# Performance work log

Measured on AMD Instinct MI355X. Metric: run time of the kernel, lower is better.

The kernel has to match this reference:

```python
import jax, jax.numpy as jnp
import numpy as np

# Problem sizes
P = 4096            # number of distinct property ids (segment domain)
N = 16_777_216      # number of value tokens in batch

# PropertyLossTracker hyperparameters (from __init__ defaults)
POWER = 0.5
EMA_DECAY = 0.99
MIN_FREQ = 1e-5
WARMUP_BATCHES = 1000
SLOW_WARMUP = 3000
MAX_WEIGHT = 30.0
RAMP_BATCHES = 200


def setup_inputs() -> dict:
    key = jax.random.key(0)
    k1, k2, k3 = jax.random.split(key, 3)
    property_ids = jax.random.randint(k1, (N,), 0, P)
    # CE-like nonnegative per-token losses
    token_losses = jax.random.uniform(k2, (N,), dtype=jnp.float32) * 5.0
    # EMA frequency state (dense vector replacing the defaultdict)
    prop_freq = jax.random.uniform(k3, (P,), dtype=jnp.float32) * 0.01 + MIN_FREQ
    return {
        "property_ids": property_ids,
        "token_losses": token_losses,
        "prop_freq": prop_freq,
        "batch_counter": 5000,  # > slow_warmup: steady-state weighting branch
    }


def reference(property_ids, token_losses, prop_freq, batch_counter):
    # --- fused segment reductions (replaces python loop over unique ids) ---
    ones = jnp.ones_like(token_losses)
    counts = jax.ops.segment_sum(ones, property_ids, num_segments=P)          # [P]
    sums = jax.ops.segment_sum(token_losses, property_ids, num_segments=P)    # [P]
    present = counts > 0
    # per-property mean loss (masked segment-mean)
    mean_loss = jnp.where(present, sums / jnp.maximum(counts, 1.0), 0.0)

    # --- EMA frequency update (decay all, add batch freq for present props) ---
    n_tokens = jnp.asarray(token_losses.shape[0], dtype=jnp.float32)
    batch_freq = counts / (n_tokens + 1e-6)
    new_freq = prop_freq * EMA_DECAY + jnp.where(present, (1.0 - EMA_DECAY) * batch_freq, 0.0)

    # --- inverse-frequency weights ---
    freq_cl = jnp.maximum(new_freq, MIN_FREQ)
    raw = 1.0 / (freq_cl + 1e-6) ** POWER
    ramp = jnp.minimum(1.0, (batch_counter - WARMUP_BATCHES) / RAMP_BATCHES)
    raw = 1.0 + ramp * (raw - 1.0)
    raw = jnp.minimum(MAX_WEIGHT, raw)
    # slow-warmup blend branch
    frac = batch_counter / SLOW_WARMUP
    raw = jnp.where(batch_counter <= SLOW_WARMUP, raw * frac + (1.0 - frac), raw)
    raw = jnp.where(batch_counter <= WARMUP_BATCHES, 1.0, raw)

    w = jnp.where(present, raw, 0.0)
    w = w / (w.sum() + 1e-6)

    stratified_loss = (mean_loss * w).sum()
    unweighted_loss = token_losses.mean()
    return stratified_loss, unweighted_loss, new_freq
```

## Files before the change

### kernel.cpp

```cpp
#include <hip/hip_runtime.h>

#define NPROP 4096
#define NTOK  16777216
#define BLOCK 256
#define NWAVES (BLOCK / 64)
#define GRID  512
#define NREP  8
#define STRIDE (GRID * BLOCK)
#define ROUNDS (NTOK / 4 / STRIDE)

#define TAG_SH 24
#define DATA_MASK 0x00FFFFFFu
#define CNT_SH 16
#define CNT_MASK 0xFFu
#define SUM_MASK 0xFFFFu
#define FXP_SCALE 32.0f
#define INV_FXP   (1.0f / 32.0f)

#define CSHIFT64 39
#define SUM_MASK64 ((1ULL << CSHIFT64) - 1)


__global__ __launch_bounds__(BLOCK) void hist_kernel(
    const int* __restrict__ ids, const float* __restrict__ losses,
    unsigned long long* __restrict__ g_rep)
{
    __shared__ unsigned s_hist[NWAVES * NPROP];
    for (int i = threadIdx.x; i < NWAVES * NPROP; i += BLOCK) s_hist[i] = 0u;
    __syncthreads();

    const int lane = threadIdx.x & 63;
    const int wave = threadIdx.x >> 6;
    unsigned* h = s_hist + wave * NPROP;

    const int4*   ids4 = (const int4*)ids;
    const float4* ls4  = (const float4*)losses;
    const int tid = blockIdx.x * BLOCK + threadIdx.x;

    int4   id = ids4[tid];
    float4 l  = ls4[tid];

    for (int b = 0; b < ROUNDS; ++b) {
        int nb = (b + 1) & (ROUNDS - 1);
        int4   idn = ids4[tid + nb * STRIDE];
        float4 ln  = ls4[tid + nb * STRIDE];

        int      bin[4] = { id.x, id.y, id.z, id.w };
        float    lv[4]  = { l.x,  l.y,  l.z,  l.w };
        unsigned contrib[4], tag[4], cur[4];

#pragma unroll
        for (int u = 0; u < 4; ++u) {
            contrib[u] = (1u << CNT_SH) | (unsigned)(lv[u] * FXP_SCALE + 0.5f);
            tag[u] = ((unsigned)((lane << 2) | u)) << TAG_SH;
            cur[u] = h[bin[u]];
        }

        unsigned pend = 0xFu;
        while (__any(pend != 0u)) {
#pragma unroll
            for (int u = 0; u < 4; ++u)
                if (pend & (1u << u))
                    h[bin[u]] = ((cur[u] & DATA_MASK) + contrib[u]) | tag[u];
#pragma unroll
            for (int u = 0; u < 4; ++u)
                if (pend & (1u << u)) {
                    unsigned chk = *(volatile unsigned*)&h[bin[u]];
                    if ((chk >> TAG_SH) == (tag[u] >> TAG_SH)) pend &= ~(1u << u);
                    else cur[u] = chk;
                }
        }

        id = idn; l = ln;
    }
    __syncthreads();

    unsigned long long* rep = g_rep + (unsigned)(blockIdx.x & (NREP - 1)) * NPROP;
    for (int i = threadIdx.x; i < NPROP; i += BLOCK) {
        unsigned c = 0, s = 0;
#pragma unroll
        for (int w = 0; w < NWAVES; ++w) {
            unsigned v = s_hist[w * NPROP + i];
            c += (v >> CNT_SH) & CNT_MASK;
            s += v & SUM_MASK;
        }
        if (c) atomicAdd(&rep[i], ((unsigned long long)c << CSHIFT64) | (unsigned long long)s);
    }
}

__global__ __launch_bounds__(1024) void finalize_kernel(
    const unsigned long long* __restrict__ g_rep,
    const float* __restrict__ prop_freq, const int* __restrict__ d_bc,
    float* __restrict__ out)
{
    __shared__ float s_raw[16], s_dot[16], s_tot[16];

    const int bc_i = d_bc[0];
    const float bc = (float)bc_i;
    const float ramp = fminf(1.0f, (bc - 1000.0f) / 200.0f);
    const float frac = bc / 3000.0f;

    float a_raw = 0.0f, a_dot = 0.0f, a_tot = 0.0f;

    for (int p = threadIdx.x; p < NPROP; p += 1024) {
        unsigned long long v = 0;
#pragma unroll
        for (int r = 0; r < NREP; ++r)
            v += g_rep[r * NPROP + p];

        float cnt  = (float)(unsigned)(v >> CSHIFT64);
        float sumf = (float)(v & SUM_MASK64) * INV_FXP;
        bool present = cnt > 0.0f;
        a_tot += sumf;

        float mean_loss = present ? sumf / fmaxf(cnt, 1.0f) : 0.0f;
        float batch_freq = cnt / ((float)NTOK + 1e-6f);
        float new_freq = prop_freq[p] * 0.99f + (present ? 0.01f * batch_freq : 0.0f);
        out[2 + p] = new_freq;

        float freq_cl = fmaxf(new_freq, 1e-5f);
        float raw = 1.0f / sqrtf(freq_cl + 1e-6f);
        raw = 1.0f + ramp * (raw - 1.0f);
        raw = fminf(30.0f, raw);
        if (bc_i <= 3000) raw = raw * frac + (1.0f - frac);
        if (bc_i <= 1000) raw = 1.0f;

        float w = present ? raw : 0.0f;
        a_raw += w;
        a_dot += mean_loss * w;
    }

    for (int off = 32; off > 0; off >>= 1) {
        a_raw += __shfl_down(a_raw, off, 64);
        a_dot += __shfl_down(a_dot, off, 64);
        a_tot += __shfl_down(a_tot, off, 64);
    }
    int wv = threadIdx.x >> 6;
    if ((threadIdx.x & 63) == 0) {
        s_raw[wv] = a_raw;
        s_dot[wv] = a_dot;
        s_tot[wv] = a_tot;
    }
    __syncthreads();
    if (threadIdx.x == 0) {
        float t_raw = 0.0f, t_dot = 0.0f, t_tot = 0.0f;
        for (int i = 0; i < 16; ++i) {
            t_raw += s_raw[i];
            t_dot += s_dot[i];
            t_tot += s_tot[i];
        }
        out[0] = t_dot / (t_raw + 1e-6f);
        out[1] = t_tot / (float)NTOK;
    }
}

extern "C" void kernel_launch(void* const* d_in, const int* in_sizes, int n_in,
                              void* d_out, int out_size, void* d_ws, size_t ws_size,
                              hipStream_t stream) {
    const int*   ids       = (const int*)d_in[0];
    const float* losses    = (const float*)d_in[1];
    const float* prop_freq = (const float*)d_in[2];
    const int*   d_bc      = (const int*)d_in[3];
    float* out = (float*)d_out;

    unsigned long long* g_rep = (unsigned long long*)d_ws;

    hipMemsetAsync(d_ws, 0, (size_t)NREP * NPROP * 8, stream);

    hist_kernel<<<GRID, BLOCK, 0, stream>>>(ids, losses, g_rep);
    finalize_kernel<<<1, 1024, 0, stream>>>(g_rep, prop_freq, d_bc, out);
}
```

Measured before the change: 178.4 us.

## Replace tagged-retry LDS loop with single attempt plus global atomic fallback

Each lane now writes its tagged update to the per-wave LDS histogram once and reads it back. Lanes whose write lost to another lane in the same wave send their contribution straight to the global replica with a 64-bit atomicAdd, so the wave-wide retry loop is gone. The load prefetch also deepens from one round ahead to two. This removes divergence and repeated LDS round trips on intra-wave bin collisions, at the cost of occasional global atomics and extra registers for the second prefetch buffer.

```diff
diff --git a/kernel.cpp b/kernel.cpp
--- a/kernel.cpp
+++ b/kernel.cpp
@@ -32,50 +32,49 @@
     const int lane = threadIdx.x & 63;
     const int wave = threadIdx.x >> 6;
     unsigned* h = s_hist + wave * NPROP;
+    unsigned long long* rep = g_rep + (unsigned)(blockIdx.x & (NREP - 1)) * NPROP;
 
     const int4*   ids4 = (const int4*)ids;
     const float4* ls4  = (const float4*)losses;
     const int tid = blockIdx.x * BLOCK + threadIdx.x;
 
-    int4   id = ids4[tid];
-    float4 l  = ls4[tid];
+    int4   idA = ids4[tid];
+    float4 lA  = ls4[tid];
+    int4   idB = ids4[tid + STRIDE];
+    float4 lB  = ls4[tid + STRIDE];
 
     for (int b = 0; b < ROUNDS; ++b) {
-        int nb = (b + 1) & (ROUNDS - 1);
-        int4   idn = ids4[tid + nb * STRIDE];
-        float4 ln  = ls4[tid + nb * STRIDE];
+        int nb = (b + 2) & (ROUNDS - 1);
+        int4   idC = ids4[tid + nb * STRIDE];
+        float4 lC  = ls4[tid + nb * STRIDE];
 
-        int      bin[4] = { id.x, id.y, id.z, id.w };
-        float    lv[4]  = { l.x,  l.y,  l.z,  l.w };
-        unsigned contrib[4], tag[4], cur[4];
+        const int      bin[4] = { idA.x, idA.y, idA.z, idA.w };
+        const float    lv[4]  = { lA.x,  lA.y,  lA.z,  lA.w };
+        unsigned contrib[4], tag8[4], cur[4], fxp[4];
 
 #pragma unroll
         for (int u = 0; u < 4; ++u) {
-            contrib[u] = (1u << CNT_SH) | (unsigned)(lv[u] * FXP_SCALE + 0.5f);
-            tag[u] = ((unsigned)((lane << 2) | u)) << TAG_SH;
+            fxp[u] = (unsigned)(lv[u] * FXP_SCALE + 0.5f);
+            contrib[u] = (1u << CNT_SH) | fxp[u];
+            tag8[u] = (unsigned)((lane << 2) | u);
             cur[u] = h[bin[u]];
         }
-
-        unsigned pend = 0xFu;
-        while (__any(pend != 0u)) {
 #pragma unroll
-            for (int u = 0; u < 4; ++u)
-                if (pend & (1u << u))
-                    h[bin[u]] = ((cur[u] & DATA_MASK) + contrib[u]) | tag[u];
+        for (int u = 0; u < 4; ++u)
+            h[bin[u]] = ((cur[u] & DATA_MASK) + contrib[u]) | (tag8[u] << TAG_SH);
 #pragma unroll
-            for (int u = 0; u < 4; ++u)
-                if (pend & (1u << u)) {
-                    unsigned chk = *(volatile unsigned*)&h[bin[u]];
-                    if ((chk >> TAG_SH) == (tag[u] >> TAG_SH)) pend &= ~(1u << u);
-                    else cur[u] = chk;
-                }
+        for (int u = 0; u < 4; ++u) {
+            unsigned chk = *(volatile unsigned*)&h[bin[u]];
+            if ((chk >> TAG_SH) != tag8[u])
+                atomicAdd(&rep[bin[u]],
+                          (1ULL << CSHIFT64) | (unsigned long long)fxp[u]);
         }
 
-        id = idn; l = ln;
+        idA = idB; lA = lB;
+        idB = idC; lB = lC;
     }
     __syncthreads();
 
-    unsigned long long* rep = g_rep + (unsigned)(blockIdx.x & (NREP - 1)) * NPROP;
     for (int i = threadIdx.x; i < NPROP; i += BLOCK) {
         unsigned c = 0, s = 0;
 #pragma unroll
```

Result: slower. 197.5 us (+10.7%).
